# Performance work log

Hardware: AMD Instinct MI355X
Metric: run time of the kernel (lower is better)

Reference implementation:

```python
import jax, jax.numpy as jnp
import numpy as np

C = 256; NH = 8; HD = C // NH; NL = 4; NP = 4; DFF = 1024
B = 8; NQ = 900
SHAPES = ((100, 100), (50, 50), (25, 25), (13, 13))
LEN = sum(h * w for h, w in SHAPES)


def setup_inputs() -> dict:
    key = jax.random.key(0)
    ks = jax.random.split(key, 16)
    s = 0.02
    d = {}
    d['tgt'] = jax.random.normal(ks[0], (B, NQ, C), jnp.float32)
    d['query_pos'] = jax.random.normal(ks[1], (B, NQ, C), jnp.float32)
    d['reference_points'] = jax.random.uniform(ks[2], (B, NQ, NL, 2), jnp.float32)
    d['src'] = jax.random.normal(ks[3], (B, LEN, C), jnp.float32)
    d['spatial_shapes'] = np.array(SHAPES, dtype=np.int32)
    # self-attn (nn.MultiheadAttention) params, stored [in,out]
    d['sa_in_w'] = jax.random.normal(ks[4], (C, 3 * C), jnp.float32) * s
    d['sa_in_b'] = jnp.zeros((3 * C,), jnp.float32)
    d['sa_out_w'] = jax.random.normal(ks[5], (C, C), jnp.float32) * s
    d['sa_out_b'] = jnp.zeros((C,), jnp.float32)
    d['ln2_g'] = jnp.ones((C,), jnp.float32); d['ln2_b'] = jnp.zeros((C,), jnp.float32)
    # MSDeformAttn params
    d['off_w'] = jax.random.normal(ks[6], (C, NH * NL * NP * 2), jnp.float32) * s
    d['off_b'] = jax.random.normal(ks[7], (NH * NL * NP * 2,), jnp.float32) * 0.5
    d['attw_w'] = jax.random.normal(ks[8], (C, NH * NL * NP), jnp.float32) * s
    d['attw_b'] = jnp.zeros((NH * NL * NP,), jnp.float32)
    d['val_w'] = jax.random.normal(ks[9], (C, C), jnp.float32) * s
    d['val_b'] = jnp.zeros((C,), jnp.float32)
    d['proj_w'] = jax.random.normal(ks[10], (C, C), jnp.float32) * s
    d['proj_b'] = jnp.zeros((C,), jnp.float32)
    d['ln1_g'] = jnp.ones((C,), jnp.float32); d['ln1_b'] = jnp.zeros((C,), jnp.float32)
    # FFN
    d['lin1_w'] = jax.random.normal(ks[11], (C, DFF), jnp.float32) * s
    d['lin1_b'] = jnp.zeros((DFF,), jnp.float32)
    d['lin2_w'] = jax.random.normal(ks[12], (DFF, C), jnp.float32) * s
    d['lin2_b'] = jnp.zeros((C,), jnp.float32)
    d['ln3_g'] = jnp.ones((C,), jnp.float32); d['ln3_b'] = jnp.zeros((C,), jnp.float32)
    return d


def _ln(x, g, b):
    m = jnp.mean(x, -1, keepdims=True)
    v = jnp.mean((x - m) ** 2, -1, keepdims=True)
    return (x - m) * jax.lax.rsqrt(v + 1e-5) * g + b


def _bilinear(v, loc, H, W):
    # v: [B,NH,H*W,HD]; loc: [B,NQ,NH,NP,2] normalized to [0,1]
    # matches F.grid_sample(align_corners=False, padding_mode='zeros')
    b = v.shape[0]; nq = loc.shape[1]
    x = loc[..., 0] * W - 0.5
    y = loc[..., 1] * H - 0.5
    x0 = jnp.floor(x); y0 = jnp.floor(y)
    dx = x - x0; dy = y - y0
    x0i = x0.astype(jnp.int32); y0i = y0.astype(jnp.int32)

    def gat(ix, iy):
        valid = ((ix >= 0) & (ix < W) & (iy >= 0) & (iy < H)).astype(v.dtype)
        idx = jnp.clip(iy, 0, H - 1) * W + jnp.clip(ix, 0, W - 1)  # [B,NQ,NH,NP]
        idx_t = jnp.transpose(idx, (0, 2, 1, 3)).reshape(b, NH, nq * NP)
        g = jnp.take_along_axis(v, idx_t[..., None], axis=2).reshape(b, NH, nq, NP, HD)
        return g * jnp.transpose(valid, (0, 2, 1, 3))[..., None]

    wt = lambda a: jnp.transpose(a, (0, 2, 1, 3))[..., None]
    return (gat(x0i, y0i) * wt((1 - dx) * (1 - dy))
            + gat(x0i + 1, y0i) * wt(dx * (1 - dy))
            + gat(x0i, y0i + 1) * wt((1 - dx) * dy)
            + gat(x0i + 1, y0i + 1) * wt(dx * dy))


def _msda(q, ref, src, shapes, val_w, val_b, off_w, off_b, attw_w, attw_b, proj_w, proj_b):
    b, nq, _ = q.shape
    value = jnp.transpose((src @ val_w + val_b).reshape(b, -1, NH, HD), (0, 2, 1, 3))  # [B,NH,Len,HD]
    off = (q @ off_w + off_b).reshape(b, nq, NH, NL, NP, 2)
    aw = jax.nn.softmax((q @ attw_w + attw_b).reshape(b, nq, NH, NL * NP), -1)
    aw = aw.reshape(b, nq, NH, NL, NP)
    acc = jnp.zeros((b, NH, nq, HD), q.dtype)
    start = 0
    for l, (H_, W_) in enumerate(shapes):
        norm = jnp.array([W_, H_], q.dtype)
        loc = ref[:, :, None, l, None, :] + off[:, :, :, l] / norm  # [B,NQ,NH,NP,2]
        smp = _bilinear(value[:, :, start:start + H_ * W_], loc, H_, W_)  # [B,NH,NQ,NP,HD]
        acc = acc + jnp.sum(smp * jnp.transpose(aw[:, :, :, l], (0, 2, 1, 3))[..., None], axis=3)
        start += H_ * W_
    out = jnp.transpose(acc, (0, 2, 1, 3)).reshape(b, nq, C)
    return out @ proj_w + proj_b


def _self_attn(x, pos, in_w, in_b, out_w, out_b):
    b, nq, _ = x.shape
    qk = x + pos
    q = (qk @ in_w[:, :C] + in_b[:C]).reshape(b, nq, NH, HD)
    k = (qk @ in_w[:, C:2 * C] + in_b[C:2 * C]).reshape(b, nq, NH, HD)
    v = (x @ in_w[:, 2 * C:] + in_b[2 * C:]).reshape(b, nq, NH, HD)
    att = jax.nn.softmax(jnp.einsum('bqhd,bkhd->bhqk', q, k) * (1.0 / float(np.sqrt(HD))), -1)
    o = jnp.einsum('bhqk,bkhd->bqhd', att, v).reshape(b, nq, C)
    return o @ out_w + out_b


def _forward(tgt, query_pos, reference_points, src, shapes,
             sa_in_w, sa_in_b, sa_out_w, sa_out_b, ln2_g, ln2_b,
             off_w, off_b, attw_w, attw_b, val_w, val_b, proj_w, proj_b, ln1_g, ln1_b,
             lin1_w, lin1_b, lin2_w, lin2_b, ln3_g, ln3_b):
    t2 = _self_attn(tgt, query_pos, sa_in_w, sa_in_b, sa_out_w, sa_out_b)
    t = _ln(tgt + t2, ln2_g, ln2_b)
    t2 = _msda(t + query_pos, reference_points, src, shapes,
               val_w, val_b, off_w, off_b, attw_w, attw_b, proj_w, proj_b)
    t = _ln(t + t2, ln1_g, ln1_b)
    h = jax.nn.relu(t @ lin1_w + lin1_b) @ lin2_w + lin2_b
    return _ln(t + h, ln3_g, ln3_b)


def reference(tgt, query_pos, reference_points, src, spatial_shapes,
              sa_in_w, sa_in_b, sa_out_w, sa_out_b, ln2_g, ln2_b,
              off_w, off_b, attw_w, attw_b, val_w, val_b, proj_w, proj_b, ln1_g, ln1_b,
              lin1_w, lin1_b, lin2_w, lin2_b, ln3_g, ln3_b):
    shapes = [(int(h), int(w)) for h, w in np.asarray(spatial_shapes)]
    return _forward(tgt, query_pos, reference_points, src, shapes,
                    sa_in_w, sa_in_b, sa_out_w, sa_out_b, ln2_g, ln2_b,
                    off_w, off_b, attw_w, attw_b, val_w, val_b, proj_w, proj_b, ln1_g, ln1_b,
                    lin1_w, lin1_b, lin2_w, lin2_b, ln3_g, ln3_b)
```

## Files before the change

kernel.cpp:

```cpp
#include <hip/hip_runtime.h>
#include <hip/hip_bf16.h>
#include <type_traits>

#define C_DIM 256
#define NHEAD 8
#define HDIM 32
#define NLVL 4
#define NPT 4
#define DFF_DIM 1024
#define BB 8
#define NQ_DIM 900
#define LEN_DIM 13294
#define ROWS (BB * NQ_DIM)
#define VROWS (BB * LEN_DIM)
#define VT_LD 928

typedef __attribute__((ext_vector_type(8))) short short8v;
typedef __attribute__((ext_vector_type(8))) unsigned short ushort8v;
typedef __attribute__((ext_vector_type(4))) float float4v;
typedef __attribute__((ext_vector_type(4))) unsigned short ushort4v;

__device__ __forceinline__ float bf2f(unsigned short u) {
  union { unsigned int i; float f; } v; v.i = ((unsigned int)u) << 16; return v.f;
}
__device__ __forceinline__ unsigned short f2bf(float f) {
  __hip_bfloat16 h = __float2bfloat16(f);
  return *reinterpret_cast<unsigned short*>(&h);
}

#define WCONV_BLOCKS 2048
__global__ __launch_bounds__(256) void wprep_kernel(
    const float* __restrict__ w0, const float* __restrict__ w1,
    const float* __restrict__ w2, const float* __restrict__ w3,
    const float* __restrict__ w4, const float* __restrict__ w5,
    const float* __restrict__ w6, const float* __restrict__ w7,
    unsigned short* __restrict__ out,
    const float* __restrict__ tgt, const float* __restrict__ qpos,
    unsigned short* __restrict__ tgtbf, unsigned short* __restrict__ x0bf, int n4) {
  int bid = blockIdx.x;
  if (bid < WCONV_BLOCKS) {
    const int Ks[8] = {256, 256, 256, 256, 256, 256, 256, 1024};
    const int Ns[8] = {768, 256, 256, 128, 256, 256, 1024, 256};
    const int Oo[8] = {0, 196608, 262144, 327680, 360448, 425984, 491520, 753664};
    int w = bid >> 8, bx = bid & 255;
    int K = Ks[w], N = Ns[w];
    int ntx = N >> 5, nty = K >> 5;
    if (bx >= ntx * nty) return;
    int tx = bx % ntx, ty = bx / ntx;
    const float* W = w == 0 ? w0 : w == 1 ? w1 : w == 2 ? w2 : w == 3 ? w3
                   : w == 4 ? w4 : w == 5 ? w5 : w == 6 ? w6 : w7;
    __shared__ float tile[32][33];
    int c = threadIdx.x & 31, rg = threadIdx.x >> 5;
#pragma unroll
    for (int j = 0; j < 4; ++j) {
      int k = ty * 32 + rg * 4 + j;
      tile[rg * 4 + j][c] = W[(size_t)k * N + tx * 32 + c];
    }
    __syncthreads();
    unsigned short* o = out + Oo[w];
#pragma unroll
    for (int j = 0; j < 4; ++j) {
      int n = tx * 32 + rg * 4 + j;
      o[(size_t)n * K + ty * 32 + c] = f2bf(tile[c][rg * 4 + j]);
    }
  } else {
    int i = (bid - WCONV_BLOCKS) * 256 + threadIdx.x;
    if (i < n4) {
      float4 x = reinterpret_cast<const float4*>(tgt)[i];
      float4 y = reinterpret_cast<const float4*>(qpos)[i];
      ushort4v u1, u2;
      u1[0] = f2bf(x.x); u1[1] = f2bf(x.y); u1[2] = f2bf(x.z); u1[3] = f2bf(x.w);
      u2[0] = f2bf(x.x + y.x); u2[1] = f2bf(x.y + y.y);
      u2[2] = f2bf(x.z + y.z); u2[3] = f2bf(x.w + y.w);
      *reinterpret_cast<ushort4v*>(tgtbf + (size_t)i * 4) = u1;
      *reinterpret_cast<ushort4v*>(x0bf + (size_t)i * 4) = u2;
    }
  }
}

template <typename TA, typename TO, int RELU>
__device__ __forceinline__ void gemm_body(
    unsigned short* smem,
    const TA* __restrict__ A, const TA* __restrict__ A2,
    const unsigned short* __restrict__ Wt,
    const float* __restrict__ bias, const float* __restrict__ bias2,
    TO* __restrict__ Cout, TO* __restrict__ Cout2,
    int M, int N, int K, int lda, int ldc, int ldc2, int colSplit,
    int bx, int by) {
  auto Al = reinterpret_cast<unsigned short(*)[128][40]>(smem);
  auto Wl = reinterpret_cast<unsigned short(*)[128][40]>(smem + 10240);
  const int tid = threadIdx.x;
  const int lane = tid & 63, wid = tid >> 6;
  const int g = lane >> 4, ql = lane & 15;
  const int wr = wid >> 1, wc = wid & 1;
  const int row0 = by * 128, col0 = bx * 128;

  const TA* Ause = (A2 != nullptr && col0 >= colSplit) ? A2 : A;

  float4v acc[4][4];
#pragma unroll
  for (int i = 0; i < 4; ++i)
#pragma unroll
    for (int j = 0; j < 4; ++j) acc[i][j] = (float4v){0.f, 0.f, 0.f, 0.f};

  float4 areg_f[4];
  ushort8v areg_b[2];
  ushort8v wreg[2];

  auto loadA = [&](int k0) {
    if constexpr (std::is_same<TA, float>::value) {
#pragma unroll
      for (int j = 0; j < 4; ++j) {
        int c = tid + 256 * j;
        int row = c >> 3, f4 = c & 7;
        int gr = min(row0 + row, M - 1);
        areg_f[j] = *reinterpret_cast<const float4*>(Ause + (size_t)gr * lda + k0 + f4 * 4);
      }
    } else {
#pragma unroll
      for (int j = 0; j < 2; ++j) {
        int c = tid + 256 * j;
        int row = c >> 2, ch = c & 3;
        int gr = min(row0 + row, M - 1);
        areg_b[j] = *reinterpret_cast<const ushort8v*>(
            reinterpret_cast<const unsigned short*>(Ause) + (size_t)gr * lda + k0 + ch * 8);
      }
    }
  };
  auto loadW = [&](int k0) {
#pragma unroll
    for (int j = 0; j < 2; ++j) {
      int c = tid + 256 * j;
      int row = c >> 2, ch = c & 3;
      wreg[j] = *reinterpret_cast<const ushort8v*>(
          Wt + (size_t)(col0 + row) * K + k0 + ch * 8);
    }
  };
  auto storeA = [&](int buf) {
    if constexpr (std::is_same<TA, float>::value) {
#pragma unroll
      for (int j = 0; j < 4; ++j) {
        int c = tid + 256 * j;
        int row = c >> 3, f4 = c & 7;
        ushort4v u;
        u[0] = f2bf(areg_f[j].x); u[1] = f2bf(areg_f[j].y);
        u[2] = f2bf(areg_f[j].z); u[3] = f2bf(areg_f[j].w);
        *reinterpret_cast<ushort4v*>(&Al[buf][row][f4 * 4]) = u;
      }
    } else {
#pragma unroll
      for (int j = 0; j < 2; ++j) {
        int c = tid + 256 * j;
        int row = c >> 2, ch = c & 3;
        *reinterpret_cast<ushort8v*>(&Al[buf][row][ch * 8]) = areg_b[j];
      }
    }
  };
  auto storeW = [&](int buf) {
#pragma unroll
    for (int j = 0; j < 2; ++j) {
      int c = tid + 256 * j;
      int row = c >> 2, ch = c & 3;
      *reinterpret_cast<ushort8v*>(&Wl[buf][row][ch * 8]) = wreg[j];
    }
  };

  const int nt = K >> 5;
  loadA(0); loadW(0);
  storeA(0); storeW(0);

  for (int t = 0; t < nt; ++t) {
    __syncthreads();
    if (t + 1 < nt) { loadA((t + 1) << 5); loadW((t + 1) << 5); }
    const int cur = t & 1;
    short8v af[4], bfr[4];
#pragma unroll
    for (int mi = 0; mi < 4; ++mi)
      af[mi] = *reinterpret_cast<const short8v*>(&Al[cur][wr * 64 + mi * 16 + ql][8 * g]);
#pragma unroll
    for (int ni = 0; ni < 4; ++ni)
      bfr[ni] = *reinterpret_cast<const short8v*>(&Wl[cur][wc * 64 + ni * 16 + ql][8 * g]);
#pragma unroll
    for (int mi = 0; mi < 4; ++mi)
#pragma unroll
      for (int ni = 0; ni < 4; ++ni)
        acc[mi][ni] = __builtin_amdgcn_mfma_f32_16x16x32_bf16(af[mi], bfr[ni], acc[mi][ni], 0, 0, 0);
    if (t + 1 < nt) { storeA(cur ^ 1); storeW(cur ^ 1); }
  }

  const bool sel2 = (Cout2 != nullptr && col0 >= colSplit);
  const float* bsrc = sel2 ? bias2 : bias;
  TO* outp = sel2 ? Cout2 : Cout;
  const int ldco = sel2 ? ldc2 : ldc;
  const int cbase = sel2 ? (col0 - colSplit) : col0;
  float bv[4];
#pragma unroll
  for (int ni = 0; ni < 4; ++ni) bv[ni] = bsrc[cbase + wc * 64 + ni * 16 + ql];
#pragma unroll
  for (int mi = 0; mi < 4; ++mi) {
#pragma unroll
    for (int r = 0; r < 4; ++r) {
      int row = row0 + wr * 64 + mi * 16 + 4 * g + r;
      if (row >= M) continue;
#pragma unroll
      for (int ni = 0; ni < 4; ++ni) {
        int col = cbase + wc * 64 + ni * 16 + ql;
        float v = acc[mi][ni][r] + bv[ni];
        if (RELU) v = fmaxf(v, 0.f);
        if constexpr (std::is_same<TO, float>::value) {
          outp[(size_t)row * ldco + col] = v;
        } else {
          outp[(size_t)row * ldco + col] = __float2bfloat16(v);
        }
      }
    }
  }
}

template <typename TA, typename TO, int RELU>
__device__ __forceinline__ void gemm_body64(
    unsigned short* smem,
    const TA* __restrict__ A, const TA* __restrict__ A2,
    const unsigned short* __restrict__ Wt,
    const float* __restrict__ bias, const float* __restrict__ bias2,
    TO* __restrict__ Cout, TO* __restrict__ Cout2,
    int M, int N, int K, int lda, int ldc, int ldc2, int colSplit,
    int bx, int by) {
  auto Al = reinterpret_cast<unsigned short(*)[64][40]>(smem);
  auto Wl = reinterpret_cast<unsigned short(*)[64][40]>(smem + 5120);
  const int tid = threadIdx.x;
  const int lane = tid & 63, wid = tid >> 6;
  const int g = lane >> 4, ql = lane & 15;
  const int wr = wid >> 1, wc = wid & 1;
  const int row0 = by * 64, col0 = bx * 64;

  const TA* Ause = (A2 != nullptr && col0 >= colSplit) ? A2 : A;

  float4v acc[2][2];
#pragma unroll
  for (int i = 0; i < 2; ++i)
#pragma unroll
    for (int j = 0; j < 2; ++j) acc[i][j] = (float4v){0.f, 0.f, 0.f, 0.f};

  float4 areg_f[2];
  ushort8v areg_b;
  ushort8v wreg;
  const int a_row = tid >> 2, a_ch = tid & 3;

  auto loadA = [&](int k0) {
    if constexpr (std::is_same<TA, float>::value) {
#pragma unroll
      for (int j = 0; j < 2; ++j) {
        int c = tid + 256 * j;
        int row = c >> 3, f4 = c & 7;
        int gr = min(row0 + row, M - 1);
        areg_f[j] = *reinterpret_cast<const float4*>(Ause + (size_t)gr * lda + k0 + f4 * 4);
      }
    } else {
      int gr = min(row0 + a_row, M - 1);
      areg_b = *reinterpret_cast<const ushort8v*>(
          reinterpret_cast<const unsigned short*>(Ause) + (size_t)gr * lda + k0 + a_ch * 8);
    }
  };
  auto loadW = [&](int k0) {
    wreg = *reinterpret_cast<const ushort8v*>(
        Wt + (size_t)(col0 + a_row) * K + k0 + a_ch * 8);
  };
  auto storeA = [&](int buf) {
    if constexpr (std::is_same<TA, float>::value) {
#pragma unroll
      for (int j = 0; j < 2; ++j) {
        int c = tid + 256 * j;
        int row = c >> 3, f4 = c & 7;
        ushort4v u;
        u[0] = f2bf(areg_f[j].x); u[1] = f2bf(areg_f[j].y);
        u[2] = f2bf(areg_f[j].z); u[3] = f2bf(areg_f[j].w);
        *reinterpret_cast<ushort4v*>(&Al[buf][row][f4 * 4]) = u;
      }
    } else {
      *reinterpret_cast<ushort8v*>(&Al[buf][a_row][a_ch * 8]) = areg_b;
    }
  };
  auto storeW = [&](int buf) {
    *reinterpret_cast<ushort8v*>(&Wl[buf][a_row][a_ch * 8]) = wreg;
  };

  const int nt = K >> 5;
  loadA(0); loadW(0);
  storeA(0); storeW(0);

  for (int t = 0; t < nt; ++t) {
    __syncthreads();
    if (t + 1 < nt) { loadA((t + 1) << 5); loadW((t + 1) << 5); }
    const int cur = t & 1;
    short8v af[2], bfr[2];
#pragma unroll
    for (int mi = 0; mi < 2; ++mi)
      af[mi] = *reinterpret_cast<const short8v*>(&Al[cur][wr * 32 + mi * 16 + ql][8 * g]);
#pragma unroll
    for (int ni = 0; ni < 2; ++ni)
      bfr[ni] = *reinterpret_cast<const short8v*>(&Wl[cur][wc * 32 + ni * 16 + ql][8 * g]);
#pragma unroll
    for (int mi = 0; mi < 2; ++mi)
#pragma unroll
      for (int ni = 0; ni < 2; ++ni)
        acc[mi][ni] = __builtin_amdgcn_mfma_f32_16x16x32_bf16(af[mi], bfr[ni], acc[mi][ni], 0, 0, 0);
    if (t + 1 < nt) { storeA(cur ^ 1); storeW(cur ^ 1); }
  }

  const bool sel2 = (Cout2 != nullptr && col0 >= colSplit);
  const float* bsrc = sel2 ? bias2 : bias;
  TO* outp = sel2 ? Cout2 : Cout;
  const int ldco = sel2 ? ldc2 : ldc;
  const int cbase = sel2 ? (col0 - colSplit) : col0;
  float bv[2];
#pragma unroll
  for (int ni = 0; ni < 2; ++ni) bv[ni] = bsrc[cbase + wc * 32 + ni * 16 + ql];
#pragma unroll
  for (int mi = 0; mi < 2; ++mi) {
#pragma unroll
    for (int r = 0; r < 4; ++r) {
      int row = row0 + wr * 32 + mi * 16 + 4 * g + r;
      if (row >= M) continue;
#pragma unroll
      for (int ni = 0; ni < 2; ++ni) {
        int col = cbase + wc * 32 + ni * 16 + ql;
        float v = acc[mi][ni][r] + bv[ni];
        if (RELU) v = fmaxf(v, 0.f);
        if constexpr (std::is_same<TO, float>::value) {
          outp[(size_t)row * ldco + col] = v;
        } else {
          outp[(size_t)row * ldco + col] = __float2bfloat16(v);
        }
      }
    }
  }
}

template <typename TA, typename TO, int RELU>
__global__ __launch_bounds__(256) void mfma_gemm64_kernel(
    const TA* __restrict__ A, const TA* __restrict__ A2,
    const unsigned short* __restrict__ Wt,
    const float* __restrict__ bias, const float* __restrict__ bias2,
    TO* __restrict__ Cout, TO* __restrict__ Cout2,
    int M, int N, int K, int lda, int ldc, int ldc2, int colSplit) {
  __shared__ unsigned short smem[10240];
  gemm_body64<TA, TO, RELU>(smem, A, A2, Wt, bias, bias2, Cout, Cout2,
                            M, N, K, lda, ldc, ldc2, colSplit,
                            blockIdx.x, blockIdx.y);
}

#define QKV_BLOCKS (6 * 57)
__global__ __launch_bounds__(256) void qkv_value_kernel(
    const unsigned short* __restrict__ x0bf, const unsigned short* __restrict__ tgtbf,
    const unsigned short* __restrict__ sa_inT, const float* __restrict__ sa_in_b,
    __hip_bfloat16* __restrict__ qkbuf, __hip_bfloat16* __restrict__ vbuf,
    const float* __restrict__ src, const unsigned short* __restrict__ valT,
    const float* __restrict__ val_b, __hip_bfloat16* __restrict__ value) {
  __shared__ unsigned short smem[20480];
  int bid = blockIdx.x;
  if (bid < QKV_BLOCKS) {
    gemm_body<unsigned short, __hip_bfloat16, 0>(
        smem, x0bf, tgtbf, sa_inT, sa_in_b, sa_in_b + 512, qkbuf, vbuf,
        ROWS, 768, 256, 256, 512, 256, 512, bid % 6, bid / 6);
  } else {
    int t = bid - QKV_BLOCKS;
    gemm_body<float, __hip_bfloat16, 0>(
        smem, src, nullptr, valT, val_b, nullptr, value, nullptr,
        VROWS, 256, 256, 256, 256, 0, 1 << 30, t & 1, t >> 1);
  }
}

__global__ __launch_bounds__(256) void vtrans_kernel(
    const unsigned short* __restrict__ vbuf, unsigned short* __restrict__ vT) {
  __shared__ unsigned short tile[32][34];
  int b = blockIdx.y;
  int ct = blockIdx.x & 7;
  int rt = blockIdx.x >> 3;
  int rl = threadIdx.x >> 3, c4 = (threadIdx.x & 7) * 4;
  int gr = min(rt * 32 + rl, NQ_DIM - 1);
  ushort4v v = *reinterpret_cast<const ushort4v*>(
      vbuf + ((size_t)(b * NQ_DIM + gr)) * 256 + ct * 32 + c4);
  tile[rl][c4] = v[0]; tile[rl][c4 + 1] = v[1];
  tile[rl][c4 + 2] = v[2]; tile[rl][c4 + 3] = v[3];
  __syncthreads();
  int cl = threadIdx.x >> 3, r4 = (threadIdx.x & 7) * 4;
  ushort4v o;
  o[0] = tile[r4][cl]; o[1] = tile[r4 + 1][cl];
  o[2] = tile[r4 + 2][cl]; o[3] = tile[r4 + 3][cl];
  *reinterpret_cast<ushort4v*>(
      vT + ((size_t)b * 256 + ct * 32 + cl) * VT_LD + rt * 32 + r4) = o;
}

__global__ __launch_bounds__(256) void ln_fused_kernel(const float* __restrict__ x,
                                                       const float* __restrict__ y,
                                                       const float* __restrict__ gg,
                                                       const float* __restrict__ bb,
                                                       float* __restrict__ out,
                                                       unsigned short* __restrict__ out2,
                                                       const float* __restrict__ qadd) {
  int row = blockIdx.x * 4 + (threadIdx.x >> 6);
  int lane = threadIdx.x & 63;
  size_t base = (size_t)row * C_DIM + lane * 4;
  float4 xv = *reinterpret_cast<const float4*>(x + base);
  float4 yv = *reinterpret_cast<const float4*>(y + base);
  float v0 = xv.x + yv.x, v1 = xv.y + yv.y, v2 = xv.z + yv.z, v3 = xv.w + yv.w;
  float s = v0 + v1 + v2 + v3;
  float s2 = v0 * v0 + v1 * v1 + v2 * v2 + v3 * v3;
#pragma unroll
  for (int o = 32; o > 0; o >>= 1) {
    s += __shfl_xor(s, o);
    s2 += __shfl_xor(s2, o);
  }
  float mean = s * (1.f / 256.f);
  float var = s2 * (1.f / 256.f) - mean * mean;
  float rstd = rsqrtf(var + 1e-5f);
  float4 gv = *reinterpret_cast<const float4*>(gg + lane * 4);
  float4 bv = *reinterpret_cast<const float4*>(bb + lane * 4);
  float r0 = (v0 - mean) * rstd * gv.x + bv.x;
  float r1 = (v1 - mean) * rstd * gv.y + bv.y;
  float r2 = (v2 - mean) * rstd * gv.z + bv.z;
  float r3 = (v3 - mean) * rstd * gv.w + bv.w;
  float4 ov; ov.x = r0; ov.y = r1; ov.z = r2; ov.w = r3;
  *reinterpret_cast<float4*>(out + base) = ov;
  if (out2) {
    float a0 = r0, a1 = r1, a2 = r2, a3 = r3;
    if (qadd) {
      float4 qv = *reinterpret_cast<const float4*>(qadd + base);
      a0 += qv.x; a1 += qv.y; a2 += qv.z; a3 += qv.w;
    }
    ushort4v u;
    u[0] = f2bf(a0); u[1] = f2bf(a1); u[2] = f2bf(a2); u[3] = f2bf(a3);
    *reinterpret_cast<ushort4v*>(out2 + base) = u;
  }
}

__global__ __launch_bounds__(256) void self_attn_mfma_kernel(
    const unsigned short* __restrict__ qk, const unsigned short* __restrict__ vT,
    unsigned short* __restrict__ out) {
  __shared__ unsigned short P_lds[4][16][32];
  const int tid = threadIdx.x;
  const int lane = tid & 63, wid = tid >> 6;
  const int g = lane >> 4, ql = lane & 15;
  const int bh = blockIdx.y;
  const int b = bh >> 3, h = bh & 7;
  const int q0 = blockIdx.x * 64 + wid * 16;
  const float scale = 0.17677669529663687f;

  const unsigned short* qk_b = qk + (size_t)b * NQ_DIM * 512;
  const int qrow = min(q0 + ql, NQ_DIM - 1);
  short8v qf = *reinterpret_cast<const short8v*>(
      qk_b + (size_t)qrow * 512 + h * HDIM + 8 * g);
  const unsigned short* kb = qk_b + 256 + h * HDIM + 8 * g;
  const unsigned short* vtb0 = vT + ((size_t)b * 256 + h * HDIM + ql) * VT_LD;
  const unsigned short* vtb1 = vtb0 + 16 * VT_LD;

  float4v o0 = {0.f, 0.f, 0.f, 0.f}, o1 = {0.f, 0.f, 0.f, 0.f};
  float m = -1e30f, lsum = 0.f;

  const int NT = 29;
  for (int kt = 0; kt < NT; ++kt) {
    const int k_base = kt * 32;
    int kr0 = min(k_base + ql, NQ_DIM - 1);
    int kr1 = min(k_base + 16 + ql, NQ_DIM - 1);
    short8v kf0 = *reinterpret_cast<const short8v*>(kb + (size_t)kr0 * 512);
    short8v kf1 = *reinterpret_cast<const short8v*>(kb + (size_t)kr1 * 512);
    float4v z = {0.f, 0.f, 0.f, 0.f};
    float4v s0 = __builtin_amdgcn_mfma_f32_16x16x32_bf16(kf0, qf, z, 0, 0, 0);
    float4v s1 = __builtin_amdgcn_mfma_f32_16x16x32_bf16(kf1, qf, z, 0, 0, 0);

    float s[8];
#pragma unroll
    for (int r = 0; r < 4; ++r) { s[r] = s0[r] * scale; s[4 + r] = s1[r] * scale; }
    if (kt == NT - 1) {
#pragma unroll
      for (int i = 0; i < 8; ++i) {
        int kk = k_base + 16 * (i >> 2) + 4 * g + (i & 3);
        if (kk >= NQ_DIM) s[i] = -1e30f;
      }
    }
    float tm = s[0];
#pragma unroll
    for (int i = 1; i < 8; ++i) tm = fmaxf(tm, s[i]);
    tm = fmaxf(tm, __shfl_xor(tm, 16));
    tm = fmaxf(tm, __shfl_xor(tm, 32));
    float mnew = fmaxf(m, tm);
    float alpha = __expf(m - mnew);
    float p[8];
    float ts = 0.f;
#pragma unroll
    for (int i = 0; i < 8; ++i) { p[i] = __expf(s[i] - mnew); ts += p[i]; }
    ts += __shfl_xor(ts, 16);
    ts += __shfl_xor(ts, 32);
    lsum = lsum * alpha + ts;
    m = mnew;

    ushort4v pp0, pp1;
#pragma unroll
    for (int r = 0; r < 4; ++r) { pp0[r] = f2bf(p[r]); pp1[r] = f2bf(p[4 + r]); }
    *reinterpret_cast<ushort4v*>(&P_lds[wid][ql][4 * g]) = pp0;
    *reinterpret_cast<ushort4v*>(&P_lds[wid][ql][16 + 4 * g]) = pp1;
    asm volatile("s_waitcnt lgkmcnt(0)" ::: "memory");
    __builtin_amdgcn_sched_barrier(0);

    o0 *= alpha;
    o1 *= alpha;

    short8v pf = *reinterpret_cast<const short8v*>(&P_lds[wid][ql][8 * g]);
    short8v vf0 = *reinterpret_cast<const short8v*>(vtb0 + k_base + 8 * g);
    short8v vf1 = *reinterpret_cast<const short8v*>(vtb1 + k_base + 8 * g);
    o0 = __builtin_amdgcn_mfma_f32_16x16x32_bf16(vf0, pf, o0, 0, 0, 0);
    o1 = __builtin_amdgcn_mfma_f32_16x16x32_bf16(vf1, pf, o1, 0, 0, 0);
  }

  float inv = 1.f / lsum;
  if (q0 + ql < NQ_DIM) {
    unsigned short* op = out + ((size_t)(b * NQ_DIM) + q0 + ql) * C_DIM + h * HDIM;
    ushort4v u0, u1;
#pragma unroll
    for (int r = 0; r < 4; ++r) { u0[r] = f2bf(o0[r] * inv); u1[r] = f2bf(o1[r] * inv); }
    *reinterpret_cast<ushort4v*>(op + 4 * g) = u0;
    *reinterpret_cast<ushort4v*>(op + 16 + 4 * g) = u1;
  }
}

__global__ __launch_bounds__(256) void msda_sample_kernel(
    const unsigned short* __restrict__ value,
    const float* __restrict__ off,
    const float* __restrict__ awlog,
    const float* __restrict__ refp,
    const int* __restrict__ shapes,
    unsigned short* __restrict__ out) {
  int g = blockIdx.x * 64 + (threadIdx.x >> 2);
  int d8 = threadIdx.x & 3;
  int h = g & 7;
  int row = g >> 3;
  int b = row / NQ_DIM;

  const float* lg = awlog + (size_t)row * 128 + h * 16;
  float aw16[16];
  float mx = -1e30f;
#pragma unroll
  for (int i = 0; i < 4; ++i) {
    float4 v = *reinterpret_cast<const float4*>(lg + i * 4);
    aw16[i * 4 + 0] = v.x; aw16[i * 4 + 1] = v.y;
    aw16[i * 4 + 2] = v.z; aw16[i * 4 + 3] = v.w;
  }
#pragma unroll
  for (int i = 0; i < 16; ++i) mx = fmaxf(mx, aw16[i]);
  float ssum = 0.f;
#pragma unroll
  for (int i = 0; i < 16; ++i) { aw16[i] = __expf(aw16[i] - mx); ssum += aw16[i]; }
  float sinv = 1.f / ssum;

  float acc[8] = {};
  int start = 0;
  const float* offr = off + (size_t)row * 256 + h * 32;
  const float* rpr  = refp + (size_t)row * NLVL * 2;
#pragma unroll
  for (int l = 0; l < NLVL; ++l) {
    int Hl = shapes[2 * l], Wl = shapes[2 * l + 1];
    float fx = rpr[2 * l + 0] * (float)Wl - 0.5f;
    float fy = rpr[2 * l + 1] * (float)Hl - 0.5f;
    const unsigned short* vbase =
        value + ((size_t)(b * LEN_DIM + start)) * C_DIM + h * HDIM + d8 * 8;
#pragma unroll
    for (int p = 0; p < NPT; ++p) {
      float x = fx + offr[l * 8 + p * 2];
      float y = fy + offr[l * 8 + p * 2 + 1];
      float a = aw16[l * 4 + p] * sinv;
      float x0f = floorf(x), y0f = floorf(y);
      float dx = x - x0f, dy = y - y0f;
      int x0 = (int)x0f, y0 = (int)y0f;
      int x1 = x0 + 1, y1 = y0 + 1;
      float wx1 = dx, wx0 = 1.f - dx;
      float wy1 = dy * a, wy0 = (1.f - dy) * a;
      bool vx0 = ((unsigned)x0 < (unsigned)Wl);
      bool vx1 = ((unsigned)x1 < (unsigned)Wl);
      bool vy0 = ((unsigned)y0 < (unsigned)Hl);
      bool vy1 = ((unsigned)y1 < (unsigned)Hl);
      float w00 = (vx0 && vy0) ? wx0 * wy0 : 0.f;
      float w10 = (vx1 && vy0) ? wx1 * wy0 : 0.f;
      float w01 = (vx0 && vy1) ? wx0 * wy1 : 0.f;
      float w11 = (vx1 && vy1) ? wx1 * wy1 : 0.f;
      int x0c = min(max(x0, 0), Wl - 1), x1c = min(max(x1, 0), Wl - 1);
      int y0c = min(max(y0, 0), Hl - 1), y1c = min(max(y1, 0), Hl - 1);
      int r0 = y0c * Wl, r1 = y1c * Wl;
      ushort8v g00 = *reinterpret_cast<const ushort8v*>(vbase + ((r0 + x0c) << 8));
      ushort8v g10 = *reinterpret_cast<const ushort8v*>(vbase + ((r0 + x1c) << 8));
      ushort8v g01 = *reinterpret_cast<const ushort8v*>(vbase + ((r1 + x0c) << 8));
      ushort8v g11 = *reinterpret_cast<const ushort8v*>(vbase + ((r1 + x1c) << 8));
#pragma unroll
      for (int j = 0; j < 8; ++j)
        acc[j] += w00 * bf2f(g00[j]) + w10 * bf2f(g10[j]) +
                  w01 * bf2f(g01[j]) + w11 * bf2f(g11[j]);
    }
    start += Hl * Wl;
  }
  ushort8v o;
#pragma unroll
  for (int j = 0; j < 8; ++j) o[j] = f2bf(acc[j]);
  *reinterpret_cast<ushort8v*>(out + (size_t)row * C_DIM + h * HDIM + d8 * 8) = o;
}

extern "C" void kernel_launch(void* const* d_in, const int* in_sizes, int n_in,
                              void* d_out, int out_size, void* d_ws, size_t ws_size,
                              hipStream_t stream) {
  const float* tgt      = (const float*)d_in[0];
  const float* qpos     = (const float*)d_in[1];
  const float* refp     = (const float*)d_in[2];
  const float* src      = (const float*)d_in[3];
  const int*   shapes   = (const int*)d_in[4];
  const float* sa_in_w  = (const float*)d_in[5];
  const float* sa_in_b  = (const float*)d_in[6];
  const float* sa_out_w = (const float*)d_in[7];
  const float* sa_out_b = (const float*)d_in[8];
  const float* ln2_g    = (const float*)d_in[9];
  const float* ln2_b    = (const float*)d_in[10];
  const float* off_w    = (const float*)d_in[11];
  const float* off_b    = (const float*)d_in[12];
  const float* attw_w   = (const float*)d_in[13];
  const float* attw_b   = (const float*)d_in[14];
  const float* val_w    = (const float*)d_in[15];
  const float* val_b    = (const float*)d_in[16];
  const float* proj_w   = (const float*)d_in[17];
  const float* proj_b   = (const float*)d_in[18];
  const float* ln1_g    = (const float*)d_in[19];
  const float* ln1_b    = (const float*)d_in[20];
  const float* lin1_w   = (const float*)d_in[21];
  const float* lin1_b   = (const float*)d_in[22];
  const float* lin2_w   = (const float*)d_in[23];
  const float* lin2_b   = (const float*)d_in[24];
  const float* ln3_g    = (const float*)d_in[25];
  const float* ln3_b    = (const float*)d_in[26];

  char* ws = (char*)d_ws;
  size_t off_b_ws = 0;
  auto alloc = [&](size_t bytes) {
    char* p = ws + off_b_ws;
    off_b_ws += (bytes + 255) & ~(size_t)255;
    return p;
  };
  unsigned short* wT     = (unsigned short*)alloc((size_t)1015808 * 2);
  unsigned short* value  = (unsigned short*)alloc((size_t)VROWS * C_DIM * 2);
  unsigned short* qkbuf  = (unsigned short*)alloc((size_t)ROWS * 512 * 2);
  unsigned short* vbuf   = (unsigned short*)alloc((size_t)ROWS * 256 * 2);
  unsigned short* vTbuf  = (unsigned short*)alloc((size_t)BB * 256 * VT_LD * 2);
  unsigned short* tgtbf  = (unsigned short*)alloc((size_t)ROWS * C_DIM * 2);
  unsigned short* X0bf   = (unsigned short*)alloc((size_t)ROWS * C_DIM * 2);
  unsigned short* attnbf = (unsigned short*)alloc((size_t)ROWS * C_DIM * 2);
  unsigned short* X3bf   = (unsigned short*)alloc((size_t)ROWS * C_DIM * 2);
  unsigned short* sampbf = (unsigned short*)alloc((size_t)ROWS * C_DIM * 2);
  unsigned short* X6bf   = (unsigned short*)alloc((size_t)ROWS * C_DIM * 2);
  unsigned short* hidbf  = (unsigned short*)alloc((size_t)ROWS * DFF_DIM * 2);
  float* X1 = (float*)alloc((size_t)ROWS * C_DIM * 4);
  float* X2 = (float*)alloc((size_t)ROWS * C_DIM * 4);
  float* X4 = (float*)alloc((size_t)ROWS * C_DIM * 4);
  float* X5 = (float*)alloc((size_t)ROWS * 128 * 4);
  float* X6 = (float*)alloc((size_t)ROWS * C_DIM * 4);
  if (off_b_ws > ws_size) return;

  unsigned short* sa_inT = wT + 0;
  unsigned short* sa_outT = wT + 196608;
  unsigned short* offT   = wT + 262144;
  unsigned short* valT   = wT + 360448;
  unsigned short* projT  = wT + 425984;
  unsigned short* lin1T  = wT + 491520;
  unsigned short* lin2T  = wT + 753664;

  dim3 blk(256);
  const int MBV = (VROWS + 127) / 128;
  const int MB64 = (ROWS + 63) / 64;
  int n4 = ROWS * C_DIM / 4;
  int prepBlocks = (n4 + 255) / 256;
  const int lnBlocks = ROWS / 4;

  wprep_kernel<<<WCONV_BLOCKS + prepBlocks, blk, 0, stream>>>(
      sa_in_w, sa_out_w, off_w, attw_w, val_w, proj_w, lin1_w, lin2_w, wT,
      tgt, qpos, tgtbf, X0bf, n4);

  qkv_value_kernel<<<QKV_BLOCKS + 2 * MBV, blk, 0, stream>>>(
      X0bf, tgtbf, sa_inT, sa_in_b, (__hip_bfloat16*)qkbuf, (__hip_bfloat16*)vbuf,
      src, valT, val_b, (__hip_bfloat16*)value);

  vtrans_kernel<<<dim3(8 * 29, BB), blk, 0, stream>>>(vbuf, vTbuf);

  self_attn_mfma_kernel<<<dim3(15, 64), blk, 0, stream>>>(qkbuf, vTbuf, attnbf);

  mfma_gemm64_kernel<unsigned short, float, 0><<<dim3(4, MB64), blk, 0, stream>>>(
      attnbf, nullptr, sa_outT, sa_out_b, nullptr,
      X1, nullptr, ROWS, 256, 256, 256, 256, 0, 1 << 30);
  ln_fused_kernel<<<lnBlocks, blk, 0, stream>>>(tgt, X1, ln2_g, ln2_b, X2, X3bf, qpos);

  mfma_gemm64_kernel<unsigned short, float, 0><<<dim3(6, MB64), blk, 0, stream>>>(
      X3bf, nullptr, offT, off_b, attw_b,
      X4, X5, ROWS, 384, 256, 256, 256, 128, 256);
  msda_sample_kernel<<<ROWS * NHEAD / 64, blk, 0, stream>>>(
      value, X4, X5, refp, shapes, sampbf);
  mfma_gemm64_kernel<unsigned short, float, 0><<<dim3(4, MB64), blk, 0, stream>>>(
      sampbf, nullptr, projT, proj_b, nullptr,
      X1, nullptr, ROWS, 256, 256, 256, 256, 0, 1 << 30);
  ln_fused_kernel<<<lnBlocks, blk, 0, stream>>>(X2, X1, ln1_g, ln1_b, X6, X6bf, nullptr);

  mfma_gemm64_kernel<unsigned short, __hip_bfloat16, 1><<<dim3(16, MB64), blk, 0, stream>>>(
      X6bf, nullptr, lin1T, lin1_b, nullptr,
      (__hip_bfloat16*)hidbf, nullptr, ROWS, 1024, 256, 256, 1024, 0, 1 << 30);
  mfma_gemm64_kernel<unsigned short, float, 0><<<dim3(4, MB64), blk, 0, stream>>>(
      hidbf, nullptr, lin2T, lin2_b, nullptr,
      X1, nullptr, ROWS, 256, 1024, 1024, 256, 0, 1 << 30);
  ln_fused_kernel<<<lnBlocks, blk, 0, stream>>>(X6, X1, ln3_g, ln3_b, (float*)d_out, nullptr, nullptr);
}
```

Baseline: 210.0 us.

## Double GEMM K-tile to 64 with XOR-swizzled LDS layout

The 128x128 GEMM body now stages K=64 slices per iteration instead of 32, which halves the number of barriers and main-loop trips. Shared memory switches from padded rows to an XOR-swizzled 128-byte row layout, meant to avoid LDS bank conflicts without padding. LDS use rises to 64KB per block and register staging doubles, which may cut occupancy for the fused QKV/value kernel.

```diff
diff --git a/kernel.cpp b/kernel.cpp
--- a/kernel.cpp
+++ b/kernel.cpp
@@ -80,15 +80,13 @@
 
 template <typename TA, typename TO, int RELU>
 __device__ __forceinline__ void gemm_body(
-    unsigned short* smem,
+    char* smem,
     const TA* __restrict__ A, const TA* __restrict__ A2,
     const unsigned short* __restrict__ Wt,
     const float* __restrict__ bias, const float* __restrict__ bias2,
     TO* __restrict__ Cout, TO* __restrict__ Cout2,
     int M, int N, int K, int lda, int ldc, int ldc2, int colSplit,
     int bx, int by) {
-  auto Al = reinterpret_cast<unsigned short(*)[128][40]>(smem);
-  auto Wl = reinterpret_cast<unsigned short(*)[128][40]>(smem + 10240);
   const int tid = threadIdx.x;
   const int lane = tid & 63, wid = tid >> 6;
   const int g = lane >> 4, ql = lane & 15;
@@ -103,24 +101,24 @@
 #pragma unroll
     for (int j = 0; j < 4; ++j) acc[i][j] = (float4v){0.f, 0.f, 0.f, 0.f};
 
-  float4 areg_f[4];
-  ushort8v areg_b[2];
-  ushort8v wreg[2];
+  float4 areg_f[8];
+  ushort8v areg_b[4];
+  ushort8v wreg[4];
 
   auto loadA = [&](int k0) {
     if constexpr (std::is_same<TA, float>::value) {
 #pragma unroll
+      for (int j = 0; j < 8; ++j) {
+        int c = tid + 256 * j;
+        int row = c >> 4, ch = c & 15;
+        int gr = min(row0 + row, M - 1);
+        areg_f[j] = *reinterpret_cast<const float4*>(Ause + (size_t)gr * lda + k0 + ch * 4);
+      }
+    } else {
+#pragma unroll
       for (int j = 0; j < 4; ++j) {
         int c = tid + 256 * j;
-        int row = c >> 3, f4 = c & 7;
-        int gr = min(row0 + row, M - 1);
-        areg_f[j] = *reinterpret_cast<const float4*>(Ause + (size_t)gr * lda + k0 + f4 * 4);
-      }
-    } else {
-#pragma unroll
-      for (int j = 0; j < 2; ++j) {
-        int c = tid + 256 * j;
-        int row = c >> 2, ch = c & 3;
+        int row = c >> 3, ch = c & 7;
         int gr = min(row0 + row, M - 1);
         areg_b[j] = *reinterpret_cast<const ushort8v*>(
             reinterpret_cast<const unsigned short*>(Ause) + (size_t)gr * lda + k0 + ch * 8);
@@ -129,63 +127,81 @@
   };
   auto loadW = [&](int k0) {
 #pragma unroll
-    for (int j = 0; j < 2; ++j) {
+    for (int j = 0; j < 4; ++j) {
       int c = tid + 256 * j;
-      int row = c >> 2, ch = c & 3;
+      int row = c >> 3, ch = c & 7;
       wreg[j] = *reinterpret_cast<const ushort8v*>(
           Wt + (size_t)(col0 + row) * K + k0 + ch * 8);
     }
   };
   auto storeA = [&](int buf) {
+    char* base = smem + buf * 16384;
     if constexpr (std::is_same<TA, float>::value) {
 #pragma unroll
-      for (int j = 0; j < 4; ++j) {
+      for (int j = 0; j < 8; ++j) {
         int c = tid + 256 * j;
-        int row = c >> 3, f4 = c & 7;
+        int row = c >> 4, ch = c & 15;
         ushort4v u;
         u[0] = f2bf(areg_f[j].x); u[1] = f2bf(areg_f[j].y);
         u[2] = f2bf(areg_f[j].z); u[3] = f2bf(areg_f[j].w);
-        *reinterpret_cast<ushort4v*>(&Al[buf][row][f4 * 4]) = u;
+        int off = row * 128 + ((ch * 8) ^ ((row & 7) << 4));
+        *reinterpret_cast<ushort4v*>(base + off) = u;
       }
     } else {
 #pragma unroll
-      for (int j = 0; j < 2; ++j) {
+      for (int j = 0; j < 4; ++j) {
         int c = tid + 256 * j;
-        int row = c >> 2, ch = c & 3;
-        *reinterpret_cast<ushort8v*>(&Al[buf][row][ch * 8]) = areg_b[j];
+        int row = c >> 3, ch = c & 7;
+        int off = row * 128 + ((ch * 16) ^ ((row & 7) << 4));
+        *reinterpret_cast<ushort8v*>(base + off) = areg_b[j];
       }
     }
   };
   auto storeW = [&](int buf) {
-#pragma unroll
-    for (int j = 0; j < 2; ++j) {
+    char* base = smem + 32768 + buf * 16384;
+#pragma unroll
+    for (int j = 0; j < 4; ++j) {
       int c = tid + 256 * j;
-      int row = c >> 2, ch = c & 3;
-      *reinterpret_cast<ushort8v*>(&Wl[buf][row][ch * 8]) = wreg[j];
-    }
-  };
-
-  const int nt = K >> 5;
+      int row = c >> 3, ch = c & 7;
+      int off = row * 128 + ((ch * 16) ^ ((row & 7) << 4));
+      *reinterpret_cast<ushort8v*>(base + off) = wreg[j];
+    }
+  };
+  auto compute = [&](int buf) {
+    const char* abase = smem + buf * 16384;
+    const char* wbase = smem + 32768 + buf * 16384;
+#pragma unroll
+    for (int kk = 0; kk < 2; ++kk) {
+      short8v af[4], bfr[4];
+#pragma unroll
+      for (int mi = 0; mi < 4; ++mi) {
+        int r = wr * 64 + mi * 16 + ql;
+        int off = r * 128 + ((kk * 64 + g * 16) ^ ((r & 7) << 4));
+        af[mi] = *reinterpret_cast<const short8v*>(abase + off);
+      }
+#pragma unroll
+      for (int ni = 0; ni < 4; ++ni) {
+        int r = wc * 64 + ni * 16 + ql;
+        int off = r * 128 + ((kk * 64 + g * 16) ^ ((r & 7) << 4));
+        bfr[ni] = *reinterpret_cast<const short8v*>(wbase + off);
+      }
+#pragma unroll
+      for (int mi = 0; mi < 4; ++mi)
+#pragma unroll
+        for (int ni = 0; ni < 4; ++ni)
+          acc[mi][ni] = __builtin_amdgcn_mfma_f32_16x16x32_bf16(af[mi], bfr[ni], acc[mi][ni], 0, 0, 0);
+    }
+  };
+
+  const int nt = K >> 6;
   loadA(0); loadW(0);
   storeA(0); storeW(0);
 
   for (int t = 0; t < nt; ++t) {
     __syncthreads();
-    if (t + 1 < nt) { loadA((t + 1) << 5); loadW((t + 1) << 5); }
-    const int cur = t & 1;
-    short8v af[4], bfr[4];
-#pragma unroll
-    for (int mi = 0; mi < 4; ++mi)
-      af[mi] = *reinterpret_cast<const short8v*>(&Al[cur][wr * 64 + mi * 16 + ql][8 * g]);
-#pragma unroll
-    for (int ni = 0; ni < 4; ++ni)
-      bfr[ni] = *reinterpret_cast<const short8v*>(&Wl[cur][wc * 64 + ni * 16 + ql][8 * g]);
-#pragma unroll
-    for (int mi = 0; mi < 4; ++mi)
-#pragma unroll
-      for (int ni = 0; ni < 4; ++ni)
-        acc[mi][ni] = __builtin_amdgcn_mfma_f32_16x16x32_bf16(af[mi], bfr[ni], acc[mi][ni], 0, 0, 0);
-    if (t + 1 < nt) { storeA(cur ^ 1); storeW(cur ^ 1); }
+    if (t + 1 < nt) { loadA((t + 1) << 6); loadW((t + 1) << 6); }
+    compute(t & 1);
+    if (t + 1 < nt) { storeA((t & 1) ^ 1); storeW((t & 1) ^ 1); }
   }
 
   const bool sel2 = (Cout2 != nullptr && col0 >= colSplit);
@@ -357,7 +373,7 @@
     __hip_bfloat16* __restrict__ qkbuf, __hip_bfloat16* __restrict__ vbuf,
     const float* __restrict__ src, const unsigned short* __restrict__ valT,
     const float* __restrict__ val_b, __hip_bfloat16* __restrict__ value) {
-  __shared__ unsigned short smem[20480];
+  __shared__ char smem[65536];
   int bid = blockIdx.x;
   if (bid < QKV_BLOCKS) {
     gemm_body<unsigned short, __hip_bfloat16, 0>(
```

New measurement: 205.6 us. -2.1%, faster.
